# Kernel tuning notes

Hardware: AMD Instinct MI355X
Metric: run time of the kernel (lower is better)

The kernel has to match this reference:

```python
import jax, jax.numpy as jnp
import numpy as np

EPS = 1e-6

def setup_inputs() -> dict:
    key = jax.random.key(0)
    k1, k2, k3 = jax.random.split(key, 3)
    B, N, F, OUT = 16, 1024, 64, 128
    x = jax.random.normal(k1, (B, N, F), dtype=jnp.float32)
    A = jax.random.uniform(k2, (B, N, N), dtype=jnp.float32)
    kernel = jax.random.normal(k3, (3 * F, OUT), dtype=jnp.float32) * 0.05
    bias = jnp.zeros((OUT,), dtype=jnp.float32)
    return {"x": x, "A": A, "kernel": kernel, "bias": bias}


def reference(x, A, kernel, bias):
    # x: [B,N,F], A: [B,N,N]
    n = A.shape[-1]
    eye = jnp.eye(n, dtype=A.dtype)
    Az = A * (1.0 - eye)          # zero out diagonal (A -= diag(diag_part(A)))
    A_hat = Az + eye              # add self-loops
    deg = A_hat.sum(axis=2)       # [B,N]
    inv_asym = 1.0 / (EPS + deg)                 # D^{-1}
    s = 1.0 / (EPS + jnp.sqrt(deg))              # D^{-1/2}
    # Three message-passing variants; apply diagonal scalings as broadcasts
    o1 = jnp.matmul(Az, x)                                   # A x
    o2 = inv_asym[:, :, None] * jnp.matmul(A_hat, x)         # D^{-1} A_hat x
    o3 = s[:, :, None] * jnp.matmul(A_hat, s[:, :, None] * x)  # D^{-1/2} A_hat D^{-1/2} x
    out = jnp.concatenate([o1, o2, o3], axis=-1)             # [B,N,3F]
    out = jnp.matmul(out, kernel) + bias                     # [B,N,OUT]
    return jax.nn.relu(out)
```

## Files before the change

### kernel.cpp

```cpp
#include <hip/hip_runtime.h>
#include <hip/hip_bf16.h>
#include <cstdint>

#define BATCH 16
#define NN    1024
#define FF    64
#define OUTF  128
#define KCAT  192
#define EPSV  1e-6f

typedef __attribute__((ext_vector_type(4))) float  f32x4;
typedef __attribute__((ext_vector_type(8))) __bf16 bf16x8;
typedef __attribute__((ext_vector_type(4))) __bf16 bf16x4;

__global__ __launch_bounds__(256) void k_deg(const float* __restrict__ A,
                                             float* __restrict__ d1,
                                             float* __restrict__ sArr) {
    int wave = threadIdx.x >> 6;
    int lane = threadIdx.x & 63;
    int row  = blockIdx.x * 4 + wave;
    const f32x4* rp = (const f32x4*)(A + (size_t)row * NN);
    float sum = 0.f;
#pragma unroll
    for (int t = 0; t < 4; ++t) {
        f32x4 v = rp[t * 64 + lane];
        sum += v[0] + v[1] + v[2] + v[3];
    }
#pragma unroll
    for (int off = 32; off; off >>= 1) sum += __shfl_xor(sum, off);
    if (lane == 0) {
        int i = row & (NN - 1);
        float diag = A[(size_t)row * NN + i];
        float deg  = 1.0f + sum - diag;
        d1[row]   = 1.0f / (EPSV + deg);
        sArr[row] = 1.0f / (EPSV + sqrtf(deg));
    }
}

__global__ __launch_bounds__(256) void k_prep(const float* __restrict__ x,
                                              const float* __restrict__ sArr,
                                              const float* __restrict__ kern,
                                              __bf16* __restrict__ xT,
                                              __bf16* __restrict__ sxT,
                                              __bf16* __restrict__ KT) {
    __shared__ float tile[64][65];
    int bid = blockIdx.x;
    int b   = bid >> 4;
    int k0  = (bid & 15) * 64;
    const float* xp = x + ((size_t)b * NN + k0) * FF;
    for (int i = threadIdx.x; i < 64 * 64; i += 256) {
        int r = i >> 6, c = i & 63;
        tile[r][c] = xp[r * FF + c];
    }
    __syncthreads();
    for (int i = threadIdx.x; i < 64 * 64; i += 256) {
        int c = i >> 6, kk = i & 63;
        float v  = tile[kk][c];
        float sv = v * sArr[b * NN + k0 + kk];
        size_t o = ((size_t)b * FF + c) * NN + k0 + kk;
        xT[o]  = (__bf16)v;
        sxT[o] = (__bf16)sv;
    }
    if (threadIdx.x < 96) {
        int idx = bid * 96 + threadIdx.x;
        int c = idx / KCAT;
        int k = idx - c * KCAT;
        KT[idx] = (__bf16)kern[k * OUTF + c];
    }
}

__global__ __launch_bounds__(512) void k_main(const float* __restrict__ A,
                                              const float* __restrict__ x,
                                              const float* __restrict__ bias,
                                              const float* __restrict__ d1g,
                                              const float* __restrict__ sg,
                                              const __bf16* __restrict__ xT,
                                              const __bf16* __restrict__ sxT,
                                              const __bf16* __restrict__ KT,
                                              float* __restrict__ out) {
    __shared__ __align__(16) float  As[64][32];
    __shared__ __align__(16) __bf16 xs[64][32];
    __shared__ __align__(16) __bf16 ss[64][32];
    __shared__ __align__(16) __bf16 os[64][192];

    const int tid  = threadIdx.x;
    const int wave = tid >> 6;
    const int lane = tid & 63;
    const int bid  = blockIdx.x;
    const int b    = bid >> 4;
    const int row0 = (bid & 15) * 64;

    const float*  Ab  = A   + (size_t)b * NN * NN;
    const __bf16* xTb = xT  + (size_t)b * FF * NN;
    const __bf16* sTb = sxT + (size_t)b * FF * NN;

    const int ar = tid >> 3;
    const int ac = (tid & 7) * 4;
    const int xc = tid >> 3;
    const int xk = (tid & 7) * 4;

    f32x4  aReg;
    bf16x4 xReg, sReg;

    auto LOAD = [&](int t) {
        int kk = t * 32;
        aReg = *(const f32x4*)(Ab + (size_t)(row0 + ar) * NN + kk + ac);
        int d = (row0 + ar) - (kk + ac);
#pragma unroll
        for (int q = 0; q < 4; ++q)
            if (d == q) aReg[q] = 0.f;
        xReg = *(const bf16x4*)(xTb + (size_t)xc * NN + kk + xk);
        sReg = *(const bf16x4*)(sTb + (size_t)xc * NN + kk + xk);
    };
    auto WRITE = [&]() {
        *(f32x4*)&As[ar][ac]  = aReg;
        *(bf16x4*)&xs[xc][xk] = xReg;
        *(bf16x4*)&ss[xc][xk] = sReg;
    };

    const int rg = wave >> 1;
    const int ch = wave & 1;
    const int l15 = lane & 15;
    const int h8  = (lane >> 4) * 8;

    f32x4 P[2] = {};
    f32x4 Q[2] = {};

    LOAD(0);
    for (int t = 0; t < 32; ++t) {
        WRITE();
        __syncthreads();
        if (t < 31) LOAD(t + 1);

        const int arow = rg * 16 + l15;
        f32x4 a0 = *(const f32x4*)&As[arow][h8];
        f32x4 a1 = *(const f32x4*)&As[arow][h8 + 4];
        bf16x8 af;
#pragma unroll
        for (int i = 0; i < 4; ++i) {
            af[i]     = (__bf16)a0[i];
            af[i + 4] = (__bf16)a1[i];
        }
#pragma unroll
        for (int g = 0; g < 2; ++g) {
            int col = ch * 32 + g * 16 + l15;
            bf16x8 xf = *(const bf16x8*)&xs[col][h8];
            bf16x8 sf = *(const bf16x8*)&ss[col][h8];
            P[g] = __builtin_amdgcn_mfma_f32_16x16x32_bf16(af, xf, P[g], 0, 0, 0);
            Q[g] = __builtin_amdgcn_mfma_f32_16x16x32_bf16(af, sf, Q[g], 0, 0, 0);
        }
        __syncthreads();
    }

#pragma unroll
    for (int j = 0; j < 4; ++j) {
        int rr   = rg * 16 + (lane >> 4) * 4 + j;
        int grow = b * NN + row0 + rr;
        float dv = d1g[grow];
        float sv = sg[grow];
#pragma unroll
        for (int g = 0; g < 2; ++g) {
            int cc = ch * 32 + g * 16 + l15;
            float xv = x[((size_t)b * NN + row0 + rr) * FF + cc];
            float o1 = P[g][j];
            float o2 = dv * (P[g][j] + xv);
            float o3 = sv * (Q[g][j] + sv * xv);
            os[rr][cc]       = (__bf16)o1;
            os[rr][64 + cc]  = (__bf16)o2;
            os[rr][128 + cc] = (__bf16)o3;
        }
    }
    __syncthreads();

    f32x4 acc[4] = {};
    const int orow = rg * 16 + l15;
#pragma unroll
    for (int ks = 0; ks < 6; ++ks) {
        bf16x8 of = *(const bf16x8*)&os[orow][ks * 32 + h8];
#pragma unroll
        for (int cg = 0; cg < 4; ++cg) {
            int col = ch * 64 + cg * 16 + l15;
            bf16x8 kf = *(const bf16x8*)&KT[(size_t)col * KCAT + ks * 32 + h8];
            acc[cg] = __builtin_amdgcn_mfma_f32_16x16x32_bf16(of, kf, acc[cg], 0, 0, 0);
        }
    }
#pragma unroll
    for (int cg = 0; cg < 4; ++cg) {
        int col  = ch * 64 + cg * 16 + l15;
        float bv = bias[col];
#pragma unroll
        for (int j = 0; j < 4; ++j) {
            int rr  = rg * 16 + (lane >> 4) * 4 + j;
            float v = acc[cg][j] + bv;
            out[((size_t)b * NN + row0 + rr) * OUTF + col] = v > 0.f ? v : 0.f;
        }
    }
}

extern "C" void kernel_launch(void* const* d_in, const int* in_sizes, int n_in,
                              void* d_out, int out_size, void* d_ws, size_t ws_size,
                              hipStream_t stream) {
    const float* x    = (const float*)d_in[0];
    const float* A    = (const float*)d_in[1];
    const float* kern = (const float*)d_in[2];
    const float* bias = (const float*)d_in[3];
    float* out = (float*)d_out;

    char* ws = (char*)d_ws;
    float*  d1  = (float*)(ws);
    float*  s   = (float*)(ws + 65536);
    __bf16* xT  = (__bf16*)(ws + 131072);
    __bf16* sxT = (__bf16*)(ws + 131072 + 2097152);
    __bf16* KT  = (__bf16*)(ws + 131072 + 2 * 2097152);
    (void)ws_size; (void)in_sizes; (void)n_in; (void)out_size;

    k_deg<<<dim3(4096), dim3(256), 0, stream>>>(A, d1, s);
    k_prep<<<dim3(256), dim3(256), 0, stream>>>(x, s, kern, xT, sxT, KT);
    k_main<<<dim3(256), dim3(512), 0, stream>>>(A, x, bias, d1, s, xT, sxT, KT, out);
}
```

Baseline: 141.9 us.

## Pre-convert diagonal-zeroed A to bf16 and stream MFMA fragments from global

The degree kernel now also zeroes the diagonal and writes A as bf16 into the workspace. The main kernel reads this half-size copy instead of fp32 A. The main kernel drops LDS staging and barriers in the K loop: each wave loads MFMA fragments straight from global memory with a 4-deep register prefetch. Tiles shrink to 16 rows across more, smaller blocks. This trades an extra 32MB write plus more re-reads of xT/sxT for less fp32 traffic in the main pass, no synchronisation, and higher occupancy.

```diff
diff --git a/kernel.cpp b/kernel.cpp
--- a/kernel.cpp
+++ b/kernel.cpp
@@ -13,25 +13,34 @@
 typedef __attribute__((ext_vector_type(8))) __bf16 bf16x8;
 typedef __attribute__((ext_vector_type(4))) __bf16 bf16x4;
 
-__global__ __launch_bounds__(256) void k_deg(const float* __restrict__ A,
-                                             float* __restrict__ d1,
-                                             float* __restrict__ sArr) {
+__global__ __launch_bounds__(256) void k_deg_cvt(const float* __restrict__ A,
+                                                 float* __restrict__ d1,
+                                                 float* __restrict__ sArr,
+                                                 __bf16* __restrict__ Az) {
     int wave = threadIdx.x >> 6;
     int lane = threadIdx.x & 63;
     int row  = blockIdx.x * 4 + wave;
+    int i    = row & (NN - 1);
     const f32x4* rp = (const f32x4*)(A + (size_t)row * NN);
+    __bf16* op = Az + (size_t)row * NN;
     float sum = 0.f;
 #pragma unroll
     for (int t = 0; t < 4; ++t) {
         f32x4 v = rp[t * 64 + lane];
+        int base = (t * 64 + lane) * 4;
+#pragma unroll
+        for (int q = 0; q < 4; ++q)
+            if (base + q == i) v[q] = 0.f;
         sum += v[0] + v[1] + v[2] + v[3];
+        bf16x4 o;
+#pragma unroll
+        for (int q = 0; q < 4; ++q) o[q] = (__bf16)v[q];
+        *(bf16x4*)(op + base) = o;
     }
 #pragma unroll
     for (int off = 32; off; off >>= 1) sum += __shfl_xor(sum, off);
     if (lane == 0) {
-        int i = row & (NN - 1);
-        float diag = A[(size_t)row * NN + i];
-        float deg  = 1.0f + sum - diag;
+        float deg = 1.0f + sum;
         d1[row]   = 1.0f / (EPSV + deg);
         sArr[row] = 1.0f / (EPSV + sqrtf(deg));
     }
@@ -69,7 +78,7 @@
     }
 }
 
-__global__ __launch_bounds__(512) void k_main(const float* __restrict__ A,
+__global__ __launch_bounds__(128) void k_main(const __bf16* __restrict__ Az,
                                               const float* __restrict__ x,
                                               const float* __restrict__ bias,
                                               const float* __restrict__ d1g,
@@ -78,120 +87,103 @@
                                               const __bf16* __restrict__ sxT,
                                               const __bf16* __restrict__ KT,
                                               float* __restrict__ out) {
-    __shared__ __align__(16) float  As[64][32];
-    __shared__ __align__(16) __bf16 xs[64][32];
-    __shared__ __align__(16) __bf16 ss[64][32];
-    __shared__ __align__(16) __bf16 os[64][192];
+    __shared__ __align__(16) __bf16 os[16][208];
 
     const int tid  = threadIdx.x;
-    const int wave = tid >> 6;
+    const int ch   = tid >> 6;
     const int lane = tid & 63;
+    const int l15  = lane & 15;
+    const int h8   = (lane >> 4) * 8;
     const int bid  = blockIdx.x;
-    const int b    = bid >> 4;
-    const int row0 = (bid & 15) * 64;
-
-    const float*  Ab  = A   + (size_t)b * NN * NN;
-    const __bf16* xTb = xT  + (size_t)b * FF * NN;
-    const __bf16* sTb = sxT + (size_t)b * FF * NN;
-
-    const int ar = tid >> 3;
-    const int ac = (tid & 7) * 4;
-    const int xc = tid >> 3;
-    const int xk = (tid & 7) * 4;
-
-    f32x4  aReg;
-    bf16x4 xReg, sReg;
-
-    auto LOAD = [&](int t) {
-        int kk = t * 32;
-        aReg = *(const f32x4*)(Ab + (size_t)(row0 + ar) * NN + kk + ac);
-        int d = (row0 + ar) - (kk + ac);
-#pragma unroll
-        for (int q = 0; q < 4; ++q)
-            if (d == q) aReg[q] = 0.f;
-        xReg = *(const bf16x4*)(xTb + (size_t)xc * NN + kk + xk);
-        sReg = *(const bf16x4*)(sTb + (size_t)xc * NN + kk + xk);
-    };
-    auto WRITE = [&]() {
-        *(f32x4*)&As[ar][ac]  = aReg;
-        *(bf16x4*)&xs[xc][xk] = xReg;
-        *(bf16x4*)&ss[xc][xk] = sReg;
-    };
-
-    const int rg = wave >> 1;
-    const int ch = wave & 1;
-    const int l15 = lane & 15;
-    const int h8  = (lane >> 4) * 8;
-
-    f32x4 P[2] = {};
-    f32x4 Q[2] = {};
-
-    LOAD(0);
-    for (int t = 0; t < 32; ++t) {
-        WRITE();
-        __syncthreads();
-        if (t < 31) LOAD(t + 1);
-
-        const int arow = rg * 16 + l15;
-        f32x4 a0 = *(const f32x4*)&As[arow][h8];
-        f32x4 a1 = *(const f32x4*)&As[arow][h8 + 4];
-        bf16x8 af;
-#pragma unroll
-        for (int i = 0; i < 4; ++i) {
-            af[i]     = (__bf16)a0[i];
-            af[i + 4] = (__bf16)a1[i];
-        }
-#pragma unroll
-        for (int g = 0; g < 2; ++g) {
-            int col = ch * 32 + g * 16 + l15;
-            bf16x8 xf = *(const bf16x8*)&xs[col][h8];
-            bf16x8 sf = *(const bf16x8*)&ss[col][h8];
-            P[g] = __builtin_amdgcn_mfma_f32_16x16x32_bf16(af, xf, P[g], 0, 0, 0);
-            Q[g] = __builtin_amdgcn_mfma_f32_16x16x32_bf16(af, sf, Q[g], 0, 0, 0);
-        }
-        __syncthreads();
-    }
+    const int b    = bid >> 6;
+    const int row0 = (bid & 63) * 16;
+
+    const __bf16* aP  = Az  + ((size_t)(b * NN + row0 + l15)) * NN + h8;
+    const __bf16* xP0 = xT  + ((size_t)(b * FF + ch * 32 + l15)) * NN + h8;
+    const __bf16* xP1 = xT  + ((size_t)(b * FF + ch * 32 + 16 + l15)) * NN + h8;
+    const __bf16* sP0 = sxT + ((size_t)(b * FF + ch * 32 + l15)) * NN + h8;
+    const __bf16* sP1 = sxT + ((size_t)(b * FF + ch * 32 + 16 + l15)) * NN + h8;
+
+    f32x4 P0 = {}, P1 = {}, Q0 = {}, Q1 = {};
+
+    bf16x8 aA, x0A, x1A, s0A, s1A;
+    bf16x8 aB, x0B, x1B, s0B, s1B;
+    bf16x8 aC, x0C, x1C, s0C, s1C;
+    bf16x8 aD, x0D, x1D, s0D, s1D;
+
+#define LOADSET(S, tt)                                          \
+    a##S  = *(const bf16x8*)(aP  + (tt) * 32);                  \
+    x0##S = *(const bf16x8*)(xP0 + (tt) * 32);                  \
+    x1##S = *(const bf16x8*)(xP1 + (tt) * 32);                  \
+    s0##S = *(const bf16x8*)(sP0 + (tt) * 32);                  \
+    s1##S = *(const bf16x8*)(sP1 + (tt) * 32);
+
+#define COMPUTE(S)                                                          \
+    P0 = __builtin_amdgcn_mfma_f32_16x16x32_bf16(a##S, x0##S, P0, 0, 0, 0); \
+    P1 = __builtin_amdgcn_mfma_f32_16x16x32_bf16(a##S, x1##S, P1, 0, 0, 0); \
+    Q0 = __builtin_amdgcn_mfma_f32_16x16x32_bf16(a##S, s0##S, Q0, 0, 0, 0); \
+    Q1 = __builtin_amdgcn_mfma_f32_16x16x32_bf16(a##S, s1##S, Q1, 0, 0, 0);
+
+    LOADSET(A, 0)
+    LOADSET(B, 1)
+    LOADSET(C, 2)
+    LOADSET(D, 3)
+#pragma unroll
+    for (int t = 0; t < 32; t += 4) {
+        COMPUTE(A) if (t + 4 < 32) { LOADSET(A, t + 4) }
+        COMPUTE(B) if (t + 5 < 32) { LOADSET(B, t + 5) }
+        COMPUTE(C) if (t + 6 < 32) { LOADSET(C, t + 6) }
+        COMPUTE(D) if (t + 7 < 32) { LOADSET(D, t + 7) }
+    }
+#undef LOADSET
+#undef COMPUTE
 
 #pragma unroll
     for (int j = 0; j < 4; ++j) {
-        int rr   = rg * 16 + (lane >> 4) * 4 + j;
+        int rr   = (lane >> 4) * 4 + j;
         int grow = b * NN + row0 + rr;
         float dv = d1g[grow];
         float sv = sg[grow];
-#pragma unroll
-        for (int g = 0; g < 2; ++g) {
-            int cc = ch * 32 + g * 16 + l15;
-            float xv = x[((size_t)b * NN + row0 + rr) * FF + cc];
-            float o1 = P[g][j];
-            float o2 = dv * (P[g][j] + xv);
-            float o3 = sv * (Q[g][j] + sv * xv);
-            os[rr][cc]       = (__bf16)o1;
-            os[rr][64 + cc]  = (__bf16)o2;
-            os[rr][128 + cc] = (__bf16)o3;
+        {
+            int cc = ch * 32 + l15;
+            float xv = x[(size_t)grow * FF + cc];
+            os[rr][cc]       = (__bf16)P0[j];
+            os[rr][64 + cc]  = (__bf16)(dv * (P0[j] + xv));
+            os[rr][128 + cc] = (__bf16)(sv * (Q0[j] + sv * xv));
         }
+        {
+            int cc = ch * 32 + 16 + l15;
+            float xv = x[(size_t)grow * FF + cc];
+            os[rr][cc]       = (__bf16)P1[j];
+            os[rr][64 + cc]  = (__bf16)(dv * (P1[j] + xv));
+            os[rr][128 + cc] = (__bf16)(sv * (Q1[j] + sv * xv));
+        }
     }
     __syncthreads();
 
-    f32x4 acc[4] = {};
-    const int orow = rg * 16 + l15;
+    f32x4 acc0 = {}, acc1 = {}, acc2 = {}, acc3 = {};
+    const int orow = l15;
 #pragma unroll
     for (int ks = 0; ks < 6; ++ks) {
         bf16x8 of = *(const bf16x8*)&os[orow][ks * 32 + h8];
-#pragma unroll
-        for (int cg = 0; cg < 4; ++cg) {
-            int col = ch * 64 + cg * 16 + l15;
-            bf16x8 kf = *(const bf16x8*)&KT[(size_t)col * KCAT + ks * 32 + h8];
-            acc[cg] = __builtin_amdgcn_mfma_f32_16x16x32_bf16(of, kf, acc[cg], 0, 0, 0);
-        }
+        bf16x8 k0 = *(const bf16x8*)&KT[(size_t)(ch * 64 + 0  + l15) * KCAT + ks * 32 + h8];
+        bf16x8 k1 = *(const bf16x8*)&KT[(size_t)(ch * 64 + 16 + l15) * KCAT + ks * 32 + h8];
+        bf16x8 k2 = *(const bf16x8*)&KT[(size_t)(ch * 64 + 32 + l15) * KCAT + ks * 32 + h8];
+        bf16x8 k3 = *(const bf16x8*)&KT[(size_t)(ch * 64 + 48 + l15) * KCAT + ks * 32 + h8];
+        acc0 = __builtin_amdgcn_mfma_f32_16x16x32_bf16(of, k0, acc0, 0, 0, 0);
+        acc1 = __builtin_amdgcn_mfma_f32_16x16x32_bf16(of, k1, acc1, 0, 0, 0);
+        acc2 = __builtin_amdgcn_mfma_f32_16x16x32_bf16(of, k2, acc2, 0, 0, 0);
+        acc3 = __builtin_amdgcn_mfma_f32_16x16x32_bf16(of, k3, acc3, 0, 0, 0);
     }
 #pragma unroll
     for (int cg = 0; cg < 4; ++cg) {
+        f32x4 av = cg == 0 ? acc0 : cg == 1 ? acc1 : cg == 2 ? acc2 : acc3;
         int col  = ch * 64 + cg * 16 + l15;
         float bv = bias[col];
 #pragma unroll
         for (int j = 0; j < 4; ++j) {
-            int rr  = rg * 16 + (lane >> 4) * 4 + j;
-            float v = acc[cg][j] + bv;
+            int rr  = (lane >> 4) * 4 + j;
+            float v = av[j] + bv;
             out[((size_t)b * NN + row0 + rr) * OUTF + col] = v > 0.f ? v : 0.f;
         }
     }
@@ -207,14 +199,15 @@
     float* out = (float*)d_out;
 
     char* ws = (char*)d_ws;
-    float*  d1  = (float*)(ws);
-    float*  s   = (float*)(ws + 65536);
-    __bf16* xT  = (__bf16*)(ws + 131072);
-    __bf16* sxT = (__bf16*)(ws + 131072 + 2097152);
-    __bf16* KT  = (__bf16*)(ws + 131072 + 2 * 2097152);
+    __bf16* Az  = (__bf16*)(ws);
+    float*  d1  = (float*)(ws + 33554432);
+    float*  s   = (float*)(ws + 33554432 + 65536);
+    __bf16* xT  = (__bf16*)(ws + 33554432 + 131072);
+    __bf16* sxT = (__bf16*)(ws + 33554432 + 131072 + 2097152);
+    __bf16* KT  = (__bf16*)(ws + 33554432 + 131072 + 2 * 2097152);
     (void)ws_size; (void)in_sizes; (void)n_in; (void)out_size;
 
-    k_deg<<<dim3(4096), dim3(256), 0, stream>>>(A, d1, s);
+    k_deg_cvt<<<dim3(4096), dim3(256), 0, stream>>>(A, d1, s, Az);
     k_prep<<<dim3(256), dim3(256), 0, stream>>>(x, s, kern, xT, sxT, KT);
-    k_main<<<dim3(256), dim3(512), 0, stream>>>(A, x, bias, d1, s, xT, sxT, KT, out);
-}
+    k_main<<<dim3(1024), dim3(128), 0, stream>>>(Az, x, bias, d1, s, xT, sxT, KT, out);
+}
```

New measurement: 153.8 us. +8.4%, slower.
